# Optimization experiments

Measured on AMD Instinct MI355X. Metric: run time of the kernel, lower is better.

The kernel has to match this reference:

```python
import jax, jax.numpy as jnp
import numpy as np

HIDDEN = 2048
HEADS = 16
HEAD_DIM = HIDDEN // HEADS
BATCH = 2
SEQ = 2048
ROPE_BASE = 10000.0


def _rope_cos_sin(seq_len, head_dim, dtype):
    inv_freq = 1.0 / (ROPE_BASE ** (jnp.arange(0, head_dim, 2, dtype=jnp.float32) / head_dim))
    t = jnp.arange(seq_len, dtype=jnp.float32)
    freqs = jnp.outer(t, inv_freq)                 # [S, D/2]
    emb = jnp.concatenate([freqs, freqs], axis=-1)  # [S, D]
    return jnp.cos(emb).astype(dtype), jnp.sin(emb).astype(dtype)


def _rotate_half(x):
    x1, x2 = jnp.split(x, 2, axis=-1)
    return jnp.concatenate([-x2, x1], axis=-1)


def setup_inputs() -> dict:
    key = jax.random.key(0)
    ks = jax.random.split(key, 5)
    scale = 1.0 / np.sqrt(HIDDEN)
    return {
        "x": jax.random.normal(ks[0], (BATCH, SEQ, HIDDEN), dtype=jnp.float32),
        "Wq": jax.random.normal(ks[1], (HIDDEN, HIDDEN), dtype=jnp.float32) * scale,
        "Wk": jax.random.normal(ks[2], (HIDDEN, HIDDEN), dtype=jnp.float32) * scale,
        "Wv": jax.random.normal(ks[3], (HIDDEN, HIDDEN), dtype=jnp.float32) * scale,
        "Wo": jax.random.normal(ks[4], (HIDDEN, HIDDEN), dtype=jnp.float32) * scale,
    }


def reference(x, Wq, Wk, Wv, Wo):
    B, S, H = x.shape
    # projections (torch Linear: y = x @ W.T)
    q = jnp.einsum('bsh,oh->bso', x, Wq).reshape(B, S, HEADS, HEAD_DIM).transpose(0, 2, 1, 3)
    k = jnp.einsum('bsh,oh->bso', x, Wk).reshape(B, S, HEADS, HEAD_DIM).transpose(0, 2, 1, 3)
    v = jnp.einsum('bsh,oh->bso', x, Wv).reshape(B, S, HEADS, HEAD_DIM).transpose(0, 2, 1, 3)
    # RoPE
    cos, sin = _rope_cos_sin(S, HEAD_DIM, x.dtype)  # [S, D]
    cos = cos[None, None]  # [1,1,S,D]
    sin = sin[None, None]
    q = q * cos + _rotate_half(q) * sin
    k = k * cos + _rotate_half(k) * sin
    # attention scores [B, H, S, S]
    scale = HEAD_DIM ** -0.5
    scores = jnp.einsum('bhqd,bhkd->bhqk', q, k) * scale
    causal = jnp.triu(jnp.ones((S, S), dtype=bool), k=1)  # kv_len==seq -> diagonal=1
    scores = jnp.where(causal[None, None], -jnp.inf, scores)
    attn = jax.nn.softmax(scores.astype(jnp.float32), axis=-1).astype(q.dtype)
    # dropout is identity in eval mode
    out = jnp.einsum('bhqk,bhkd->bhqd', attn, v)  # [B,H,S,D]
    out = out.transpose(0, 2, 1, 3).reshape(B, S, H)
    return jnp.einsum('bsh,oh->bso', out, Wo)
```

## Files before the change

kernel.cpp:

```cpp
#include <hip/hip_runtime.h>
#include <hip/hip_bf16.h>
#include <cstdint>
#include <cstddef>

constexpr int HIDDEN = 2048;
constexpr int HEADS  = 16;
constexpr int HD     = 128;
constexpr int BATCH  = 2;
constexpr int SEQ    = 2048;
constexpr int MROWS  = BATCH * SEQ;

typedef __attribute__((ext_vector_type(8))) short bf16x8;
typedef __attribute__((ext_vector_type(4))) float f32x4;
typedef __attribute__((ext_vector_type(4))) unsigned u32x4;

__device__ __forceinline__ unsigned short f2bf(float f) {
  union { float f; unsigned int u; } c; c.f = f;
  unsigned int r = c.u + 0x7FFFu + ((c.u >> 16) & 1u);
  return (unsigned short)(r >> 16);
}
__device__ __forceinline__ float bf2f(unsigned short u) {
  union { unsigned int u; float f; } c; c.u = ((unsigned int)u) << 16;
  return c.f;
}

__device__ __forceinline__ void gload_lds16(const void* g, void* l) {
  __builtin_amdgcn_global_load_lds(
      (const __attribute__((address_space(1))) void*)g,
      (__attribute__((address_space(3))) void*)l, 16, 0, 0);
}

__global__ void k_cvt_all(const float* __restrict__ x,
                          const float* __restrict__ w0, const float* __restrict__ w1,
                          const float* __restrict__ w2, const float* __restrict__ w3,
                          unsigned short* __restrict__ out) {
  constexpr int N4X = MROWS * HIDDEN / 4;
  constexpr int N4W = HIDDEN * HIDDEN / 4;
  int idx = blockIdx.x * 256 + threadIdx.x;
  const float* src;
  int off;
  if (idx < N4X) { src = x; off = idx; }
  else {
    int j = idx - N4X;
    int seg = j >> 20;
    off = j & (N4W - 1);
    src = (seg == 0) ? w0 : (seg == 1) ? w1 : (seg == 2) ? w2 : w3;
  }
  float4 v = reinterpret_cast<const float4*>(src)[off];
  ushort4 o;
  o.x = f2bf(v.x); o.y = f2bf(v.y); o.z = f2bf(v.z); o.w = f2bf(v.w);
  reinterpret_cast<ushort4*>(out)[idx] = o;
}

constexpr int GK  = 2048;
constexpr int GNT = GK / 64;

template<int MODE, int BM, int BN>
__global__ __launch_bounds__(512)
__attribute__((amdgpu_waves_per_eu(2)))
void k_gemm256(const unsigned short* __restrict__ A,
               const unsigned short* __restrict__ Bm,
               void* __restrict__ Cout) {
  constexpr int ABYTES = BM * 64 * 2;
  constexpr int BBYTES = BN * 64 * 2;
  constexpr int AG = BM / 64;
  constexpr int BG = BN / 64;
  constexpr int G  = AG + BG;
  constexpr int MI = BM / 32;
  constexpr int NI = BN / 64;

  __shared__ char lds[2 * (ABYTES + BBYTES)];
  char* ldsA = lds;
  char* ldsB = lds + 2 * ABYTES;

  const int t    = threadIdx.x;
  const int lane = t & 63;
  const int w    = t >> 6;
  const int wr   = w >> 2;
  const int wc   = w & 3;
  const int l15  = lane & 15, lg = lane >> 4;

  const int orig = blockIdx.x;
  const int wg   = (orig & 7) * 32 + (orig >> 3);
  const int m0   = (wg >> 4) * BM;
  const int n0   = (wg & 15) * BN;

  const int rowA = t >> 3;
  const int xsel = ((t & 7) ^ (rowA & 7)) * 8;
  const unsigned short* aS = A  + (size_t)(m0 + rowA) * GK + xsel;
  const unsigned short* bS = Bm + (size_t)(n0 + rowA) * GK + xsel;
  char* aD = ldsA + t * 16;
  char* bD = ldsB + t * 16;

#define STAGEG(buf, kt) do {                                       \
    const unsigned short* ap = aS + (kt) * 64;                     \
    const unsigned short* bp = bS + (kt) * 64;                     \
    char* ad = aD + (buf) * ABYTES;                                \
    char* bd = bD + (buf) * BBYTES;                                \
    _Pragma("unroll")                                              \
    for (int g = 0; g < AG; ++g)                                   \
      gload_lds16(ap + (size_t)g * 64 * GK, ad + g * 8192);        \
    _Pragma("unroll")                                              \
    for (int g = 0; g < BG; ++g)                                   \
      gload_lds16(bp + (size_t)g * 64 * GK, bd + g * 8192);        \
  } while (0)

  const int xr  = (l15 & 7) << 4;
  const int vo0 = (lg * 16) ^ xr;
  const int vo1 = (64 + lg * 16) ^ xr;
  const char* aR = ldsA + wr * (BM / 2) * 128 + l15 * 128;
  const char* bR = ldsB + wc * (BN / 4) * 128 + l15 * 128;

  f32x4 acc[MI][NI];
#pragma unroll
  for (int mi = 0; mi < MI; ++mi)
#pragma unroll
    for (int ni = 0; ni < NI; ++ni)
#pragma unroll
      for (int r = 0; r < 4; ++r) acc[mi][ni][r] = 0.f;

  STAGEG(0, 0);
  STAGEG(1, 1);
  asm volatile("s_waitcnt vmcnt(%0)" :: "i"(G) : "memory");
  __builtin_amdgcn_s_barrier();
  asm volatile("" ::: "memory");

#pragma unroll 1
  for (int kt = 0; kt < GNT; ++kt) {
    const int buf = kt & 1;
    const char* a = aR + buf * ABYTES;
    const char* b = bR + buf * BBYTES;

    bf16x8 af0[MI], bf0[NI];
#pragma unroll
    for (int mi = 0; mi < MI; ++mi)
      af0[mi] = *reinterpret_cast<const bf16x8*>(a + mi * 2048 + vo0);
#pragma unroll
    for (int ni = 0; ni < NI; ++ni)
      bf0[ni] = *reinterpret_cast<const bf16x8*>(b + ni * 2048 + vo0);
    __builtin_amdgcn_s_setprio(1);
#pragma unroll
    for (int mi = 0; mi < MI; ++mi)
#pragma unroll
      for (int ni = 0; ni < NI; ++ni)
        acc[mi][ni] = __builtin_amdgcn_mfma_f32_16x16x32_bf16(af0[mi], bf0[ni], acc[mi][ni], 0, 0, 0);
    __builtin_amdgcn_s_setprio(0);

    bf16x8 af1[MI], bf1[NI];
#pragma unroll
    for (int mi = 0; mi < MI; ++mi)
      af1[mi] = *reinterpret_cast<const bf16x8*>(a + mi * 2048 + vo1);
#pragma unroll
    for (int ni = 0; ni < NI; ++ni)
      bf1[ni] = *reinterpret_cast<const bf16x8*>(b + ni * 2048 + vo1);

    asm volatile("s_waitcnt lgkmcnt(0)" ::: "memory");
    __builtin_amdgcn_s_barrier();
    asm volatile("" ::: "memory");

    if (kt < GNT - 2) STAGEG(buf, kt + 2);

    __builtin_amdgcn_s_setprio(1);
#pragma unroll
    for (int mi = 0; mi < MI; ++mi)
#pragma unroll
      for (int ni = 0; ni < NI; ++ni)
        acc[mi][ni] = __builtin_amdgcn_mfma_f32_16x16x32_bf16(af1[mi], bf1[ni], acc[mi][ni], 0, 0, 0);
    __builtin_amdgcn_s_setprio(0);

    if (kt < GNT - 2) asm volatile("s_waitcnt vmcnt(%0)" :: "i"(G) : "memory");
    else              asm volatile("s_waitcnt vmcnt(0)" ::: "memory");
    __builtin_amdgcn_s_barrier();
    asm volatile("" ::: "memory");
  }
#undef STAGEG

#pragma unroll
  for (int mi = 0; mi < MI; ++mi) {
#pragma unroll
    for (int ni = 0; ni < NI; ++ni) {
#pragma unroll
      for (int r = 0; r < 4; ++r) {
        int row = m0 + wr * (BM / 2) + mi * 16 + lg * 4 + r;
        int col = n0 + wc * (BN / 4) + ni * 16 + l15;
        float v = acc[mi][ni][r];
        if (MODE == 2) {
          reinterpret_cast<float*>(Cout)[(size_t)row * 2048 + col] = v;
        } else if (MODE == 0) {
          int bb = row >> 11, s = row & (SEQ - 1);
          int which = col >> 11;
          int hc = col & 2047;
          int h = hc >> 7, d = hc & (HD - 1);
          size_t addr = (size_t)which * ((size_t)MROWS * HIDDEN)
                      + ((size_t)(bb * HEADS + h) * SEQ + s) * HD + d;
          reinterpret_cast<unsigned short*>(Cout)[addr] = f2bf(v);
        } else {
          int h = row >> 7, d = row & (HD - 1);
          int bb = col >> 11, s = col & (SEQ - 1);
          size_t addr = ((size_t)(bb * HEADS + h) * HD + d) * SEQ + s;
          reinterpret_cast<unsigned short*>(Cout)[addr] = f2bf(v);
        }
      }
    }
  }
}

constexpr float QSCALE = 0.08838834764831845f * 1.4426950408889634f;

__global__ void k_rope(unsigned short* __restrict__ Qb, unsigned short* __restrict__ Kb) {
  int idx = blockIdx.x * 256 + threadIdx.x;
  int c  = idx & 7;
  int s  = (idx >> 3) & (SEQ - 1);
  int bh = idx >> 14;
  size_t base = ((size_t)bh * SEQ + s) * HD + c * 8;

  bf16x8 ql = *reinterpret_cast<const bf16x8*>(Qb + base);
  bf16x8 qh = *reinterpret_cast<const bf16x8*>(Qb + base + 64);
  bf16x8 kl = *reinterpret_cast<const bf16x8*>(Kb + base);
  bf16x8 kh = *reinterpret_cast<const bf16x8*>(Kb + base + 64);
  bf16x8 qlo, qho, klo, kho;
#pragma unroll
  for (int j = 0; j < 8; ++j) {
    float d   = (float)(c * 8 + j);
    float ang = (float)s * expf(d * -0.14391156511756683f);
    float sn, cs;
    __sincosf(ang, &sn, &cs);
    float a0 = bf2f((unsigned short)ql[j]), a1 = bf2f((unsigned short)qh[j]);
    qlo[j] = (short)f2bf((a0 * cs - a1 * sn) * QSCALE);
    qho[j] = (short)f2bf((a1 * cs + a0 * sn) * QSCALE);
    float b0 = bf2f((unsigned short)kl[j]), b1 = bf2f((unsigned short)kh[j]);
    klo[j] = (short)f2bf(b0 * cs - b1 * sn);
    kho[j] = (short)f2bf(b1 * cs + b0 * sn);
  }
  *reinterpret_cast<bf16x8*>(Qb + base)      = qlo;
  *reinterpret_cast<bf16x8*>(Qb + base + 64) = qho;
  *reinterpret_cast<bf16x8*>(Kb + base)      = klo;
  *reinterpret_cast<bf16x8*>(Kb + base + 64) = kho;
}

constexpr int QB  = 128;
constexpr int KVB = 64;
constexpr int NQT = SEQ / QB;

__global__ __launch_bounds__(512)
__attribute__((amdgpu_waves_per_eu(4, 4)))
void k_attn(const unsigned short* __restrict__ Q,
            const unsigned short* __restrict__ Kk,
            const unsigned short* __restrict__ Vt,
            unsigned short* __restrict__ O) {
  __shared__ char lds[2 * 16384 + 2 * 16384];
  char* Ks = lds;
  char* Vs = lds + 2 * 16384;

  const int t    = threadIdx.x;
  const int lane = t & 63;
  const int w    = t >> 6;
  const int l15  = lane & 15, lg = lane >> 4;

  const int lin     = blockIdx.x + 16 * blockIdx.y;
  const int pos     = lin >> 3;
  const int logical = (lin & 7) * 64 + pos;
  const int bh      = logical >> 4;
  const int qt0     = logical & 15;
  const int qt      = (pos < 32) ? qt0 : (15 - qt0);
  const int b  = bh >> 4, h = bh & 15;
  const int q0b  = qt * QB;
  const int q0w  = q0b + w * 16;
  const int qw_hi = q0w + 15;

  const unsigned short* Qb = Q  + (size_t)bh * SEQ * HD;
  const unsigned short* Kb = Kk + (size_t)bh * SEQ * HD;
  const unsigned short* Vb = Vt + (size_t)bh * HD * SEQ;

  bf16x8 qf[4];
#pragma unroll
  for (int c = 0; c < 4; ++c)
    qf[c] = *reinterpret_cast<const bf16x8*>(Qb + (size_t)(q0w + l15) * HD + c * 32 + lg * 8);

  float m = -1e30f, lpart = 0.f;
  f32x4 oacc[8];
#pragma unroll
  for (int dt = 0; dt < 8; ++dt)
#pragma unroll
    for (int r = 0; r < 4; ++r) oacc[dt][r] = 0.f;

  const int sp     = t * 16;
  const int srow   = sp >> 8;
  const int scolb  = (sp & 255) ^ ((srow & 7) << 4);
  const unsigned short* ksrc2 = Kb + (size_t)srow * HD + (scolb >> 1);
  char* kdst2 = Ks + sp;

  const int vrow  = t >> 3;
  const int vcolb = ((t & 7) << 4) ^ ((vrow & 7) << 4);
  const unsigned short* vsrc = Vb + (size_t)vrow * SEQ + (vcolb >> 1);
  char* vdst = Vs + t * 16;

  const int nb = q0b / KVB + 2;

  gload_lds16(ksrc2, kdst2);
  gload_lds16(ksrc2 + (size_t)32 * HD, kdst2 + 8192);
  gload_lds16(vsrc, vdst);
  gload_lds16(vsrc + (size_t)64 * SEQ, vdst + 8192);
  __syncthreads();

  int cur = 0;
  for (int kb = 0; kb < nb; ++kb) {
    const int kv0 = kb * KVB;
    if (kb + 1 < nb) {
      const int nxt = kv0 + KVB;
      char* nk = kdst2 + (cur ^ 1) * 16384;
      char* nv = vdst  + (cur ^ 1) * 16384;
      gload_lds16(ksrc2 + (size_t)nxt * HD, nk);
      gload_lds16(ksrc2 + (size_t)(nxt + 32) * HD, nk + 8192);
      gload_lds16(vsrc + nxt, nv);
      gload_lds16(vsrc + (size_t)64 * SEQ + nxt, nv + 8192);
    }

    if (kv0 <= qw_hi) {
      const char* Kc = Ks + cur * 16384;
      const char* Vc = Vs + cur * 16384;
      f32x4 sc[4];
#pragma unroll
      for (int tt = 0; tt < 4; ++tt)
#pragma unroll
        for (int r = 0; r < 4; ++r) sc[tt][r] = 0.f;
      __builtin_amdgcn_s_setprio(1);
#pragma unroll
      for (int tt = 0; tt < 4; ++tt) {
        const int kr = tt * 16 + l15;
        const int xr = (kr & 7) << 4;
#pragma unroll
        for (int c = 0; c < 4; ++c) {
          bf16x8 kf = *reinterpret_cast<const bf16x8*>(
              Kc + kr * 256 + ((c * 64 + lg * 16) ^ xr));
          sc[tt] = __builtin_amdgcn_mfma_f32_16x16x32_bf16(kf, qf[c], sc[tt], 0, 0, 0);
        }
      }
      __builtin_amdgcn_s_setprio(0);

      const bool full = (kv0 + KVB - 1 <= q0w);
      const int qg = q0w + l15;
      if (!full) {
        const int kvb = kv0 + lg * 4;
#pragma unroll
        for (int tt = 0; tt < 4; ++tt)
#pragma unroll
          for (int r = 0; r < 4; ++r)
            if (kvb + tt * 16 + r > qg) sc[tt][r] = -1e30f;
      }
      float pm01 = fmaxf(fmaxf(sc[0][0], sc[0][1]), fmaxf(sc[0][2], sc[0][3]));
      float pm11 = fmaxf(fmaxf(sc[1][0], sc[1][1]), fmaxf(sc[1][2], sc[1][3]));
      float pm21 = fmaxf(fmaxf(sc[2][0], sc[2][1]), fmaxf(sc[2][2], sc[2][3]));
      float pm31 = fmaxf(fmaxf(sc[3][0], sc[3][1]), fmaxf(sc[3][2], sc[3][3]));
      float pm = fmaxf(fmaxf(pm01, pm11), fmaxf(pm21, pm31));
      if (__any(pm > m + 11.5f)) {
        float pmr = pm;
        pmr = fmaxf(pmr, __shfl_xor(pmr, 16));
        pmr = fmaxf(pmr, __shfl_xor(pmr, 32));
        float mn = fmaxf(m, pmr);
        float al = exp2f(m - mn);
        lpart *= al;
#pragma unroll
        for (int r = 0; r < 4; ++r) {
          float alr = __shfl(al, lg * 4 + r, 16);
#pragma unroll
          for (int dt = 0; dt < 8; ++dt) oacc[dt][r] *= alr;
        }
        m = mn;
      }
      float p[4][4];
      float ps = 0.f;
#pragma unroll
      for (int tt = 0; tt < 4; ++tt)
#pragma unroll
        for (int r = 0; r < 4; ++r) {
          p[tt][r] = exp2f(sc[tt][r] - m);
          ps += p[tt][r];
        }
      lpart += ps;

      unsigned cc[4][2];
#pragma unroll
      for (int tt = 0; tt < 4; ++tt) {
        asm("v_cvt_pk_bf16_f32 %0, %1, %2" : "=v"(cc[tt][0]) : "v"(p[tt][0]), "v"(p[tt][1]));
        asm("v_cvt_pk_bf16_f32 %0, %1, %2" : "=v"(cc[tt][1]) : "v"(p[tt][2]), "v"(p[tt][3]));
      }
      u32x4 u0, u1;
      {
        unsigned a0 = cc[0][0], b0 = cc[1][0];
        asm("v_permlane32_swap_b32 %0, %1" : "+v"(a0), "+v"(b0));
        asm("v_permlane16_swap_b32 %0, %1" : "+v"(a0), "+v"(b0));
        unsigned a1 = cc[0][1], b1 = cc[1][1];
        asm("v_permlane32_swap_b32 %0, %1" : "+v"(a1), "+v"(b1));
        asm("v_permlane16_swap_b32 %0, %1" : "+v"(a1), "+v"(b1));
        u0[0] = a0; u0[1] = a1; u0[2] = b0; u0[3] = b1;
        unsigned a2 = cc[2][0], b2 = cc[3][0];
        asm("v_permlane32_swap_b32 %0, %1" : "+v"(a2), "+v"(b2));
        asm("v_permlane16_swap_b32 %0, %1" : "+v"(a2), "+v"(b2));
        unsigned a3 = cc[2][1], b3 = cc[3][1];
        asm("v_permlane32_swap_b32 %0, %1" : "+v"(a3), "+v"(b3));
        asm("v_permlane16_swap_b32 %0, %1" : "+v"(a3), "+v"(b3));
        u1[0] = a2; u1[1] = a3; u1[2] = b2; u1[3] = b3;
      }
      bf16x8 pa0 = __builtin_bit_cast(bf16x8, u0);
      bf16x8 pa1 = __builtin_bit_cast(bf16x8, u1);

      const int xv = (l15 & 7) << 4;
      __builtin_amdgcn_s_setprio(1);
#pragma unroll
      for (int dt = 0; dt < 8; ++dt) {
        const char* vrl = Vc + (dt * 16 + l15) * 128;
        bf16x8 vf0 = *reinterpret_cast<const bf16x8*>(vrl + ((lg * 16) ^ xv));
        bf16x8 vf1 = *reinterpret_cast<const bf16x8*>(vrl + ((64 + lg * 16) ^ xv));
        oacc[dt] = __builtin_amdgcn_mfma_f32_16x16x32_bf16(pa0, vf0, oacc[dt], 0, 0, 0);
        oacc[dt] = __builtin_amdgcn_mfma_f32_16x16x32_bf16(pa1, vf1, oacc[dt], 0, 0, 0);
      }
      __builtin_amdgcn_s_setprio(0);
    }
    __syncthreads();
    cur ^= 1;
  }

  float ls = lpart;
  ls += __shfl_xor(ls, 16);
  ls += __shfl_xor(ls, 32);
  float inv = 1.0f / ls;
  float invr[4];
#pragma unroll
  for (int r = 0; r < 4; ++r) invr[r] = __shfl(inv, lg * 4 + r, 16);
#pragma unroll
  for (int dt = 0; dt < 8; ++dt) {
#pragma unroll
    for (int r = 0; r < 4; ++r) {
      int qg = q0w + lg * 4 + r;
      int dv = dt * 16 + l15;
      O[((size_t)(b * SEQ + qg) * HEADS + h) * HD + dv] = f2bf(oacc[dt][r] * invr[r]);
    }
  }
}

extern "C" void kernel_launch(void* const* d_in, const int* in_sizes, int n_in,
                              void* d_out, int out_size, void* d_ws, size_t ws_size,
                              hipStream_t stream) {
  (void)in_sizes; (void)n_in; (void)out_size; (void)ws_size;
  const float* x  = (const float*)d_in[0];
  const float* Wq = (const float*)d_in[1];
  const float* Wk = (const float*)d_in[2];
  const float* Wv = (const float*)d_in[3];
  const float* Wo = (const float*)d_in[4];
  float* out = (float*)d_out;

  unsigned short* xb  = (unsigned short*)d_ws;
  unsigned short* wqb = xb  + (size_t)MROWS * HIDDEN;
  unsigned short* wkb = wqb + (size_t)HIDDEN * HIDDEN;
  unsigned short* wvb = wkb + (size_t)HIDDEN * HIDDEN;
  unsigned short* wob = wvb + (size_t)HIDDEN * HIDDEN;
  unsigned short* Qb  = wob + (size_t)HIDDEN * HIDDEN;
  unsigned short* Kb  = Qb  + (size_t)MROWS * HIDDEN;
  unsigned short* Vtb = Kb  + (size_t)MROWS * HIDDEN;
  unsigned short* Ob  = Vtb + (size_t)MROWS * HIDDEN;
  (void)wkb;

  constexpr int CVT_THREADS = (MROWS * HIDDEN + 4 * HIDDEN * HIDDEN) / 4;
  k_cvt_all<<<CVT_THREADS / 256, 256, 0, stream>>>(x, Wq, Wk, Wv, Wo, xb);

  k_gemm256<0, 256, 256><<<256, 512, 0, stream>>>(xb, wqb, Qb);
  k_gemm256<3, 128, 256><<<256, 512, 0, stream>>>(wvb, xb, Vtb);

  k_rope<<<(BATCH * HEADS * SEQ * 8) / 256, 256, 0, stream>>>(Qb, Kb);

  k_attn<<<dim3(SEQ / QB, BATCH * HEADS), 512, 0, stream>>>(Qb, Kb, Vtb, Ob);

  k_gemm256<2, 256, 128><<<256, 512, 0, stream>>>(Ob, wob, out);
}
```

Baseline: 232.9 us.

## Fuse RoPE and Q scaling into QK projection GEMM epilogue via LDS exchange

Removes the separate RoPE kernel and applies rotary embedding and the Q softmax scale inside the Q/K projection GEMM epilogue. Partner half-dimension values held by a neighbouring wave are swapped through LDS in two halves, with barriers around each. This avoids re-reading and re-writing the Q and K tensors in global memory and saves one launch. In exchange it adds LDS traffic, synchronization and sincos work to the GEMM epilogue, and it relies on the wave-to-column mapping pairing d with d+64.

```diff
diff --git a/kernel.cpp b/kernel.cpp
--- a/kernel.cpp
+++ b/kernel.cpp
@@ -13,6 +13,8 @@
 typedef __attribute__((ext_vector_type(8))) short bf16x8;
 typedef __attribute__((ext_vector_type(4))) float f32x4;
 typedef __attribute__((ext_vector_type(4))) unsigned u32x4;
+
+constexpr float QSCALE = 0.08838834764831845f * 1.4426950408889634f;
 
 __device__ __forceinline__ unsigned short f2bf(float f) {
   union { float f; unsigned int u; } c; c.f = f;
@@ -175,67 +177,70 @@
   }
 #undef STAGEG
 
-#pragma unroll
-  for (int mi = 0; mi < MI; ++mi) {
-#pragma unroll
-    for (int ni = 0; ni < NI; ++ni) {
-#pragma unroll
-      for (int r = 0; r < 4; ++r) {
-        int row = m0 + wr * (BM / 2) + mi * 16 + lg * 4 + r;
-        int col = n0 + wc * (BN / 4) + ni * 16 + l15;
-        float v = acc[mi][ni][r];
-        if (MODE == 2) {
-          reinterpret_cast<float*>(Cout)[(size_t)row * 2048 + col] = v;
-        } else if (MODE == 0) {
-          int bb = row >> 11, s = row & (SEQ - 1);
-          int which = col >> 11;
-          int hc = col & 2047;
-          int h = hc >> 7, d = hc & (HD - 1);
-          size_t addr = (size_t)which * ((size_t)MROWS * HIDDEN)
-                      + ((size_t)(bb * HEADS + h) * SEQ + s) * HD + d;
-          reinterpret_cast<unsigned short*>(Cout)[addr] = f2bf(v);
-        } else {
-          int h = row >> 7, d = row & (HD - 1);
-          int bb = col >> 11, s = col & (SEQ - 1);
-          size_t addr = ((size_t)(bb * HEADS + h) * HD + d) * SEQ + s;
-          reinterpret_cast<unsigned short*>(Cout)[addr] = f2bf(v);
+  if (MODE == 0) {
+    float* xch = reinterpret_cast<float*>(lds);
+    const int xo = w * 4096 + lane * 64;
+    const int xw = (w ^ 1) * 4096 + lane * 64;
+#pragma unroll
+    for (int half = 0; half < 2; ++half) {
+      __syncthreads();
+#pragma unroll
+      for (int mi4 = 0; mi4 < 4; ++mi4)
+#pragma unroll
+        for (int ni = 0; ni < NI; ++ni)
+#pragma unroll
+          for (int r = 0; r < 4; ++r)
+            xch[xo + mi4 * 16 + ni * 4 + r] = acc[half * 4 + mi4][ni][r];
+      __syncthreads();
+#pragma unroll
+      for (int mi4 = 0; mi4 < 4; ++mi4) {
+#pragma unroll
+        for (int ni = 0; ni < NI; ++ni) {
+          const int col  = n0 + wc * 64 + ni * 16 + l15;
+          const float invf = expf((float)(col & 63) * -0.14391156511756683f);
+#pragma unroll
+          for (int r = 0; r < 4; ++r) {
+            int row = m0 + wr * 128 + (half * 4 + mi4) * 16 + lg * 4 + r;
+            int s = row & (SEQ - 1);
+            float own = acc[half * 4 + mi4][ni][r];
+            float oth = xch[xw + mi4 * 16 + ni * 4 + r];
+            float sn, cs;
+            __sincosf((float)s * invf, &sn, &cs);
+            float outv = (wc & 1) ? (own * cs + oth * sn) : (own * cs - oth * sn);
+            int bb = row >> 11;
+            int which = col >> 11;
+            int hc = col & 2047;
+            int h = hc >> 7, d = hc & (HD - 1);
+            if (which == 0) outv *= QSCALE;
+            size_t addr = (size_t)which * ((size_t)MROWS * HIDDEN)
+                        + ((size_t)(bb * HEADS + h) * SEQ + s) * HD + d;
+            reinterpret_cast<unsigned short*>(Cout)[addr] = f2bf(outv);
+          }
+        }
+      }
+    }
+  } else {
+#pragma unroll
+    for (int mi = 0; mi < MI; ++mi) {
+#pragma unroll
+      for (int ni = 0; ni < NI; ++ni) {
+#pragma unroll
+        for (int r = 0; r < 4; ++r) {
+          int row = m0 + wr * (BM / 2) + mi * 16 + lg * 4 + r;
+          int col = n0 + wc * (BN / 4) + ni * 16 + l15;
+          float v = acc[mi][ni][r];
+          if (MODE == 2) {
+            reinterpret_cast<float*>(Cout)[(size_t)row * 2048 + col] = v;
+          } else {
+            int h = row >> 7, d = row & (HD - 1);
+            int bb = col >> 11, s = col & (SEQ - 1);
+            size_t addr = ((size_t)(bb * HEADS + h) * HD + d) * SEQ + s;
+            reinterpret_cast<unsigned short*>(Cout)[addr] = f2bf(v);
+          }
         }
       }
     }
   }
-}
-
-constexpr float QSCALE = 0.08838834764831845f * 1.4426950408889634f;
-
-__global__ void k_rope(unsigned short* __restrict__ Qb, unsigned short* __restrict__ Kb) {
-  int idx = blockIdx.x * 256 + threadIdx.x;
-  int c  = idx & 7;
-  int s  = (idx >> 3) & (SEQ - 1);
-  int bh = idx >> 14;
-  size_t base = ((size_t)bh * SEQ + s) * HD + c * 8;
-
-  bf16x8 ql = *reinterpret_cast<const bf16x8*>(Qb + base);
-  bf16x8 qh = *reinterpret_cast<const bf16x8*>(Qb + base + 64);
-  bf16x8 kl = *reinterpret_cast<const bf16x8*>(Kb + base);
-  bf16x8 kh = *reinterpret_cast<const bf16x8*>(Kb + base + 64);
-  bf16x8 qlo, qho, klo, kho;
-#pragma unroll
-  for (int j = 0; j < 8; ++j) {
-    float d   = (float)(c * 8 + j);
-    float ang = (float)s * expf(d * -0.14391156511756683f);
-    float sn, cs;
-    __sincosf(ang, &sn, &cs);
-    float a0 = bf2f((unsigned short)ql[j]), a1 = bf2f((unsigned short)qh[j]);
-    qlo[j] = (short)f2bf((a0 * cs - a1 * sn) * QSCALE);
-    qho[j] = (short)f2bf((a1 * cs + a0 * sn) * QSCALE);
-    float b0 = bf2f((unsigned short)kl[j]), b1 = bf2f((unsigned short)kh[j]);
-    klo[j] = (short)f2bf(b0 * cs - b1 * sn);
-    kho[j] = (short)f2bf(b1 * cs + b0 * sn);
-  }
-  *reinterpret_cast<bf16x8*>(Qb + base)      = qlo;
-  *reinterpret_cast<bf16x8*>(Qb + base + 64) = qho;
-  *reinterpret_cast<bf16x8*>(Kb + base)      = klo;
-  *reinterpret_cast<bf16x8*>(Kb + base + 64) = kho;
 }
 
 constexpr int QB  = 128;
@@ -467,8 +472,6 @@
   k_gemm256<0, 256, 256><<<256, 512, 0, stream>>>(xb, wqb, Qb);
   k_gemm256<3, 128, 256><<<256, 512, 0, stream>>>(wvb, xb, Vtb);
 
-  k_rope<<<(BATCH * HEADS * SEQ * 8) / 256, 256, 0, stream>>>(Qb, Kb);
-
   k_attn<<<dim3(SEQ / QB, BATCH * HEADS), 512, 0, stream>>>(Qb, Kb, Vtb, Ob);
 
   k_gemm256<2, 256, 128><<<256, 512, 0, stream>>>(Ob, wob, out);
```

After: 231.0 us. Within noise of the previous version (-0.8%).
